# Kernel tuning notes

Hardware: AMD Instinct MI355X
Metric: run time of the kernel (lower is better)

The kernel has to match this reference:

```python
import jax, jax.numpy as jnp
import numpy as np

N_EMBED = 384
N_HEAD = 6
HEAD_SIZE = N_EMBED // N_HEAD  # 64
LN_EPS = 1e-5


def setup_inputs() -> dict:
    key = jax.random.key(0)
    ks = jax.random.split(key, 12)
    B, T = 128, 256
    s_in = 1.0 / np.sqrt(N_EMBED)
    s_ff = 1.0 / np.sqrt(4 * N_EMBED)
    return {
        "x": jax.random.normal(ks[0], (B, T, N_EMBED), jnp.float32),
        "Wq": jax.random.normal(ks[1], (N_HEAD, N_EMBED, HEAD_SIZE), jnp.float32) * s_in,
        "Wk": jax.random.normal(ks[2], (N_HEAD, N_EMBED, HEAD_SIZE), jnp.float32) * s_in,
        "Wv": jax.random.normal(ks[3], (N_HEAD, N_EMBED, HEAD_SIZE), jnp.float32) * s_in,
        "Wproj": jax.random.normal(ks[4], (N_EMBED, N_EMBED), jnp.float32) * s_in,
        "bproj": jnp.zeros((N_EMBED,), jnp.float32),
        "W1": jax.random.normal(ks[5], (N_EMBED, 4 * N_EMBED), jnp.float32) * s_in,
        "b1": jnp.zeros((4 * N_EMBED,), jnp.float32),
        "W2": jax.random.normal(ks[6], (4 * N_EMBED, N_EMBED), jnp.float32) * s_ff,
        "b2": jnp.zeros((N_EMBED,), jnp.float32),
        "ln1_g": jnp.ones((N_EMBED,), jnp.float32),
        "ln1_b": jnp.zeros((N_EMBED,), jnp.float32),
        "ln2_g": jnp.ones((N_EMBED,), jnp.float32),
        "ln2_b": jnp.zeros((N_EMBED,), jnp.float32),
    }


def _layernorm(x, g, b):
    mu = jnp.mean(x, axis=-1, keepdims=True)
    var = jnp.mean(jnp.square(x - mu), axis=-1, keepdims=True)
    return (x - mu) * jax.lax.rsqrt(var + LN_EPS) * g + b


def _attention(xn, Wq, Wk, Wv, Wproj, bproj):
    B, T, C = xn.shape
    q = jnp.einsum("btc,hcd->bhtd", xn, Wq)
    k = jnp.einsum("btc,hcd->bhtd", xn, Wk)
    v = jnp.einsum("btc,hcd->bhtd", xn, Wv)
    # NOTE: original scales by C**-0.5 with C = n_embed (384), not head_size
    scores = jnp.einsum("bhtd,bhsd->bhts", q, k) * (C ** -0.5)
    causal = jnp.tril(jnp.ones((T, T), bool))
    scores = jnp.where(causal, scores, -jnp.inf)
    wei = jax.nn.softmax(scores, axis=-1)
    out = jnp.einsum("bhts,bhsd->bhtd", wei, v)
    out = out.transpose(0, 2, 1, 3).reshape(B, T, N_EMBED)  # concat heads
    return out @ Wproj + bproj


def reference(x, Wq, Wk, Wv, Wproj, bproj, W1, b1, W2, b2, ln1_g, ln1_b, ln2_g, ln2_b):
    x = x + _attention(_layernorm(x, ln1_g, ln1_b), Wq, Wk, Wv, Wproj, bproj)
    h = _layernorm(x, ln2_g, ln2_b)
    ff = jax.nn.relu(h @ W1 + b1) @ W2 + b2
    return x + ff
```

## Files before the change

### kernel.cpp

```cpp
#include <hip/hip_runtime.h>
#include <hip/hip_bf16.h>

typedef __hip_bfloat16 bf16;
typedef __attribute__((ext_vector_type(8))) short bf16x8;
typedef __attribute__((ext_vector_type(4))) float f32x4;

#define CEMB 384
#define NHEAD 6
#define HSZ 64
#define TSEQ 256
#define BATCH 128
#define MROWS (BATCH*TSEQ)
#define FDIM 1536
#define QSCALE 0.05103103630798288f
#define SMAX 8.0f

#define AS1 __attribute__((address_space(1)))
#define AS3 __attribute__((address_space(3)))
__device__ __forceinline__ void gload16(const void* g, void* l){
  __builtin_amdgcn_global_load_lds((const AS1 unsigned*)(g), (AS3 unsigned*)(l), 16, 0, 0);
}
__device__ __forceinline__ float b2f(unsigned short u){
  unsigned int xi = ((unsigned int)u)<<16; float f; __builtin_memcpy(&f,&xi,4); return f;
}

__global__ __launch_bounds__(256) void ln_kernel(const float* __restrict__ x,
    const float* __restrict__ gam, const float* __restrict__ bet,
    bf16* __restrict__ y)
{
  const int row  = blockIdx.x*4 + (threadIdx.x>>6);
  const int lane = threadIdx.x & 63;
  const float* xr = x + (size_t)row*CEMB;
  float v[6]; float s = 0.f;
  #pragma unroll
  for (int i=0;i<6;i++){ v[i] = xr[lane + i*64]; s += v[i]; }
  #pragma unroll
  for (int m=1;m<64;m<<=1) s += __shfl_xor(s, m, 64);
  const float mu = s * (1.0f/CEMB);
  float qs = 0.f;
  #pragma unroll
  for (int i=0;i<6;i++){ v[i] -= mu; qs += v[i]*v[i]; }
  #pragma unroll
  for (int m=1;m<64;m<<=1) qs += __shfl_xor(qs, m, 64);
  const float rs = rsqrtf(qs*(1.0f/CEMB) + 1e-5f);
  bf16* yr = y + (size_t)row*CEMB;
  #pragma unroll
  for (int i=0;i<6;i++){
    int c = lane + i*64;
    yr[c] = __float2bfloat16(v[i]*rs*gam[c] + bet[c]);
  }
}

__global__ __launch_bounds__(256) void ln_kernel_b(const bf16* __restrict__ x,
    const float* __restrict__ gam, const float* __restrict__ bet,
    bf16* __restrict__ y)
{
  const int row  = blockIdx.x*4 + (threadIdx.x>>6);
  const int lane = threadIdx.x & 63;
  const ushort2* xr = (const ushort2*)(x + (size_t)row*CEMB);
  float v[6]; float s = 0.f;
  #pragma unroll
  for (int i=0;i<3;i++){
    ushort2 u = xr[lane + i*64];
    v[2*i]   = b2f(u.x); v[2*i+1] = b2f(u.y);
    s += v[2*i] + v[2*i+1];
  }
  #pragma unroll
  for (int m=1;m<64;m<<=1) s += __shfl_xor(s, m, 64);
  const float mu = s * (1.0f/CEMB);
  float qs = 0.f;
  #pragma unroll
  for (int i=0;i<6;i++){ v[i] -= mu; qs += v[i]*v[i]; }
  #pragma unroll
  for (int m=1;m<64;m<<=1) qs += __shfl_xor(qs, m, 64);
  const float rs = rsqrtf(qs*(1.0f/CEMB) + 1e-5f);
  bf16* yr = y + (size_t)row*CEMB;
  #pragma unroll
  for (int i=0;i<3;i++)
    #pragma unroll
    for (int j=0;j<2;j++){
      int c = (lane + i*64)*2 + j;
      yr[c] = __float2bfloat16(v[2*i+j]*rs*gam[c] + bet[c]);
    }
}

__global__ __launch_bounds__(256) void transpose_to_bf16(const float* __restrict__ src,
    bf16* __restrict__ dst, int K, int N)
{
  __shared__ float tile[32][33];
  const int n0 = blockIdx.x*32, k0 = blockIdx.y*32;
  src += (size_t)blockIdx.z*K*N;
  dst += (size_t)blockIdx.z*K*N;
  const int c = threadIdx.x & 31, r8 = threadIdx.x >> 5;
  #pragma unroll
  for (int i=0;i<4;i++)
    tile[r8 + i*8][c] = src[(size_t)(k0 + r8 + i*8)*N + n0 + c];
  __syncthreads();
  #pragma unroll
  for (int i=0;i<4;i++)
    dst[(size_t)(n0 + r8 + i*8)*K + k0 + c] = __float2bfloat16(tile[c][r8 + i*8]);
}

__global__ __launch_bounds__(256) void transpose_qkv(const float* __restrict__ Wq,
    const float* __restrict__ Wk, const float* __restrict__ Wv, bf16* __restrict__ dst)
{
  __shared__ float tile[32][33];
  const int z = blockIdx.z;
  const float* src = (z < 6) ? Wq : (z < 12 ? Wk : Wv);
  src += (size_t)(z % 6) * CEMB * HSZ;
  dst += (size_t)z * CEMB * HSZ;
  const int n0 = blockIdx.x*32, k0 = blockIdx.y*32;
  const int c = threadIdx.x & 31, r8 = threadIdx.x >> 5;
  #pragma unroll
  for (int i=0;i<4;i++)
    tile[r8 + i*8][c] = src[(size_t)(k0 + r8 + i*8)*HSZ + n0 + c];
  __syncthreads();
  #pragma unroll
  for (int i=0;i<4;i++)
    dst[(size_t)(n0 + r8 + i*8)*CEMB + k0 + c] = __float2bfloat16(tile[c][r8 + i*8]);
}

template<int EPI, int NN, int NK>
__global__ __launch_bounds__(512) void gemm2(
    const bf16* __restrict__ A, const bf16* __restrict__ BT,
    const float* __restrict__ bias, const float* __restrict__ resid,
    float* __restrict__ outf, bf16* __restrict__ outb0,
    bf16* __restrict__ outb1, bf16* __restrict__ outb2)
{
  constexpr int K = NK*32;
  constexpr int N = NN*128;
  __shared__ char lA[2][256*64];
  __shared__ char lB[2][128*64];
  const int cpx = gridDim.x >> 3;
  const int wg  = (blockIdx.x & 7)*cpx + (blockIdx.x >> 3);
  const int bm = (wg / NN)*256, bn = (wg % NN)*128;
  const int t = threadIdx.x, lane = t & 63, wid = t >> 6;
  const int wr = (wid>>1)*64, wc = (wid&1)*64;
  const int g = lane >> 4, fr = lane & 15;
  const size_t rowK2 = (size_t)K*2;
  f32x4 acc[4][4] = {};

  auto stage = [&](int buf, int kt){
    const size_t ko = (size_t)kt*64;
    #pragma unroll
    for (int i=0;i<2;i++){
      int slot = t + i*512;
      int row = slot>>2, blk = slot&3;
      gload16((const char*)A + (size_t)(bm+row)*rowK2 + ko + ((blk ^ ((row>>1)&3))<<4),
              lA[buf] + slot*16);
    }
    {
      int row = t>>2, blk = t&3;
      gload16((const char*)BT + (size_t)(bn+row)*rowK2 + ko + ((blk ^ ((row>>1)&3))<<4),
              lB[buf] + t*16);
    }
  };

  stage(0, 0);
  __syncthreads();
  int cur = 0;
  #pragma unroll 1
  for (int kt=0; kt<NK; ++kt){
    if (kt+1 < NK) stage(cur^1, kt+1);
    bf16x8 af[4], bq[4];
    #pragma unroll
    for (int mi=0;mi<4;mi++){
      int row = wr + mi*16 + fr;
      af[mi] = *(const bf16x8*)(lA[cur] + row*64 + ((g ^ ((row>>1)&3))<<4));
    }
    #pragma unroll
    for (int nj=0;nj<4;nj++){
      int row = wc + nj*16 + fr;
      bq[nj] = *(const bf16x8*)(lB[cur] + row*64 + ((g ^ ((row>>1)&3))<<4));
    }
    __builtin_amdgcn_s_setprio(1);
    #pragma unroll
    for (int mi=0;mi<4;mi++)
      #pragma unroll
      for (int nj=0;nj<4;nj++)
        acc[mi][nj] = __builtin_amdgcn_mfma_f32_16x16x32_bf16(af[mi], bq[nj], acc[mi][nj], 0, 0, 0);
    __builtin_amdgcn_s_setprio(0);
    __syncthreads();
    cur ^= 1;
  }

  if constexpr (EPI==0){
    const int sel = bn/CEMB;
    bf16* dst = sel==0 ? outb0 : (sel==1 ? outb1 : outb2);
    const float sc = sel==0 ? QSCALE : 1.0f;
    const int nb = bn - sel*CEMB;
    #pragma unroll
    for (int nj=0;nj<4;nj++){
      const int nn = nb + wc + nj*16 + fr;
      const int hh = nn>>6, dd = nn&63;
      #pragma unroll
      for (int mi=0;mi<4;mi++){
        const int m0 = bm + wr + mi*16 + 4*g;
        const int bb = m0>>8, tt0 = m0&255;
        bf16* p = dst + ((size_t)(bb*NHEAD + hh)*TSEQ + tt0)*HSZ + dd;
        #pragma unroll
        for (int e=0;e<4;e++)
          p[(size_t)e*HSZ] = __float2bfloat16(acc[mi][nj][e]*sc);
      }
    }
  } else {
    #pragma unroll
    for (int mi=0;mi<4;mi++)
      #pragma unroll
      for (int nj=0;nj<4;nj++)
        #pragma unroll
        for (int e=0;e<4;e++){
          const int m = bm + wr + mi*16 + 4*g + e;
          const int n = bn + wc + nj*16 + fr;
          const float vacc = acc[mi][nj][e];
          if constexpr (EPI==1){
            outb0[(size_t)m*N + n] = __float2bfloat16(vacc + bias[n] + resid[(size_t)m*N + n]);
          } else {
            float z = vacc + bias[n];
            outb0[(size_t)m*N + n] = __float2bfloat16(z > 0.f ? z : 0.f);
          }
        }
  }
}

template<int EPI, int NREAL, int NPAD, int NK>
__global__ __launch_bounds__(512, 2) void gemm8p(
    const bf16* __restrict__ A, const bf16* __restrict__ BT,
    const float* __restrict__ bias, const bf16* __restrict__ residb,
    float* __restrict__ outf)
{
  constexpr int K = NK*64;
  constexpr int NT = NPAD/256;
  __shared__ char lds[131072];
  const int cpx = gridDim.x >> 3;
  const int wg  = (blockIdx.x & 7)*cpx + (blockIdx.x >> 3);
  const int bm = (wg / NT)*256, bn = (wg % NT)*256;
  const int t = threadIdx.x, lane = t & 63, wid = t >> 6;
  const int wm = wid >> 2, wn = wid & 3;
  const int g = lane >> 4, fr = lane & 15;
  const size_t rowb = (size_t)K*2;
  const int sblk = ((t&3) ^ ((t>>3)&3)) << 4;
  const int swz  = (g ^ ((fr>>1)&3)) << 4;
  f32x4 acc[8][4] = {};

  const char* Ag = (const char*)A  + (size_t)(bm + (t>>2))*rowb + sblk;
  const char* Bg = (const char*)BT + (size_t)(bn + (t>>2))*rowb + sblk;
  const size_t rstep = rowb*128;

  auto stg = [&](int X, int KH, int sl, int kt2){
    const char* src = (X ? Bg : Ag) + (size_t)kt2*128 + KH*64;
    char* dst = lds + X*65536 + (KH*2+sl)*16384 + wid*1024;
    gload16(src,         dst);
    gload16(src + rstep, dst + 8192);
  };
  auto rdA = [&](bf16x8* af, int sl, int MH, int KS){
    const char* p = lds + (KS*2+sl)*16384 + (wm*128 + MH*64 + fr)*64 + swz;
    #pragma unroll
    for (int mi=0;mi<4;mi++) af[mi] = *(const bf16x8*)(p + mi*1024);
  };
  auto rdB = [&](bf16x8* bq, int sl, int KS){
    const char* p = lds + 65536 + (KS*2+sl)*16384 + (wn*64 + fr)*64 + swz;
    #pragma unroll
    for (int nj=0;nj<4;nj++) bq[nj] = *(const bf16x8*)(p + nj*1024);
  };

#define MFMA16(MH) \
  __builtin_amdgcn_s_setprio(1); \
  _Pragma("unroll") \
  for (int mi=0;mi<4;mi++){ \
    _Pragma("unroll") \
    for (int nj=0;nj<4;nj++) \
      acc[(MH)*4+mi][nj] = __builtin_amdgcn_mfma_f32_16x16x32_bf16(af[mi], bq[nj], acc[(MH)*4+mi][nj], 0, 0, 0); \
  } \
  __builtin_amdgcn_s_setprio(0);

  stg(0,0,0,0); stg(1,0,0,0); stg(0,1,0,0); stg(1,1,0,0);
  asm volatile("s_waitcnt vmcnt(4)" ::: "memory");
  __builtin_amdgcn_s_barrier();

  #pragma unroll 1
  for (int kt=0; kt<NK; ++kt){
    const int sl = kt&1, sn = sl^1;
    const bool pf = (kt+1 < NK);
    bf16x8 af[4], bq[4];
    rdA(af, sl, 0, 0); rdB(bq, sl, 0);
    if (pf) stg(0,0,sn,kt+1);
    __builtin_amdgcn_s_barrier();
    asm volatile("s_waitcnt lgkmcnt(0)" ::: "memory");
    __builtin_amdgcn_sched_barrier(0);
    MFMA16(0)
    __builtin_amdgcn_s_barrier();
    rdA(af, sl, 1, 0);
    if (pf){ stg(1,0,sn,kt+1);
             asm volatile("s_waitcnt vmcnt(4)" ::: "memory"); }
    else     asm volatile("s_waitcnt vmcnt(0)" ::: "memory");
    __builtin_amdgcn_s_barrier();
    asm volatile("s_waitcnt lgkmcnt(0)" ::: "memory");
    __builtin_amdgcn_sched_barrier(0);
    MFMA16(1)
    __builtin_amdgcn_s_barrier();
    rdA(af, sl, 0, 1); rdB(bq, sl, 1);
    if (pf) stg(0,1,sn,kt+1);
    __builtin_amdgcn_s_barrier();
    asm volatile("s_waitcnt lgkmcnt(0)" ::: "memory");
    __builtin_amdgcn_sched_barrier(0);
    MFMA16(0)
    __builtin_amdgcn_s_barrier();
    rdA(af, sl, 1, 1);
    if (pf){ stg(1,1,sn,kt+1);
             asm volatile("s_waitcnt vmcnt(4)" ::: "memory"); }
    __builtin_amdgcn_s_barrier();
    asm volatile("s_waitcnt lgkmcnt(0)" ::: "memory");
    __builtin_amdgcn_sched_barrier(0);
    MFMA16(1)
    __builtin_amdgcn_s_barrier();
  }
#undef MFMA16

  #pragma unroll
  for (int mi=0;mi<8;mi++)
    #pragma unroll
    for (int nj=0;nj<4;nj++)
      #pragma unroll
      for (int e=0;e<4;e++){
        const int m = bm + wm*128 + mi*16 + 4*g + e;
        const int n = bn + wn*64 + nj*16 + fr;
        if (NPAD == NREAL || n < NREAL){
          const float vacc = acc[mi][nj][e];
          outf[(size_t)m*NREAL + n] = vacc + bias[n] +
              b2f(*(const unsigned short*)&residb[(size_t)m*NREAL + n]);
        }
      }
}

__global__ __launch_bounds__(256) void attn_kernel(
    const bf16* __restrict__ q, const bf16* __restrict__ k,
    const bf16* __restrict__ v, bf16* __restrict__ out)
{
  __shared__ char kt_lds[64*128];
  __shared__ char vt_lds[80*128];
  __shared__ char p_lds[4][64*128];
  const int bh = blockIdx.x;
  const int bidx = bh / NHEAD, hidx = bh - bidx*NHEAD;
  const int t = threadIdx.x, lane = t & 63, w = t >> 6;
  const int g = lane >> 4, fr = lane & 15;
  const int lrow = lane >> 3;
  const int scol = ((lane & 7) ^ lrow) << 4;
  const size_t base = (size_t)bh * TSEQ * HSZ;

  if (t < 128){
    unsigned int ones2 = 0x3F803F80u;
    uint4 vv;
    if ((t>>3) == 0) vv = uint4{ones2, ones2, ones2, ones2};
    else             vv = uint4{0u, 0u, 0u, 0u};
    *(uint4*)(vt_lds + (64 + (t>>3))*128 + (t&7)*16) = vv;
  }

  bf16x8 qf[4][2];
  #pragma unroll
  for (int mi=0;mi<4;mi++)
    #pragma unroll
    for (int ks=0;ks<2;ks++)
      qf[mi][ks] = *(const bf16x8*)(q + base + (size_t)(w*64 + mi*16 + fr)*HSZ + ks*32 + g*8);

  f32x4 of[4][5] = {};

  for (int j=0;j<4;j++){
    __syncthreads();
    #pragma unroll
    for (int i=0;i<2;i++){
      int r0 = w*16 + i*8;
      gload16((const char*)(k + base + (size_t)(j*64 + r0 + lrow)*HSZ) + scol,
              kt_lds + r0*128);
    }
    #pragma unroll
    for (int i=0;i<2;i++){
      int chunk = t + i*256, r = chunk>>3, c = chunk&7;
      uint4 vv = *(const uint4*)(v + base + (size_t)(j*64 + r)*HSZ + c*8);
      const unsigned short* pv = (const unsigned short*)&vv;
      #pragma unroll
      for (int u=0;u<8;u++)
        *(unsigned short*)(vt_lds + (c*8+u)*128 + ((((r>>3) ^ u ^ c)&7)<<4) + (r&7)*2) = pv[u];
    }
    __syncthreads();
    if (j <= w){
      f32x4 sa[4][4] = {};
      #pragma unroll
      for (int ks=0;ks<2;ks++){
        bf16x8 kf[4];
        #pragma unroll
        for (int nj=0;nj<4;nj++)
          kf[nj] = *(const bf16x8*)(kt_lds + (nj*16+fr)*128 + (((ks*4+g)*16) ^ ((fr&7)<<4)));
        __builtin_amdgcn_s_setprio(1);
        #pragma unroll
        for (int mi=0;mi<4;mi++)
          #pragma unroll
          for (int nj=0;nj<4;nj++)
            sa[mi][nj] = __builtin_amdgcn_mfma_f32_16x16x32_bf16(qf[mi][ks], kf[nj], sa[mi][nj], 0, 0, 0);
        __builtin_amdgcn_s_setprio(0);
      }
      if (j == w){
        #pragma unroll
        for (int mi=0;mi<4;mi++)
          #pragma unroll
          for (int nj=0;nj<4;nj++)
            #pragma unroll
            for (int e=0;e<4;e++)
              if (nj*16 + fr > mi*16 + 4*g + e) sa[mi][nj][e] = -1e30f;
      }
      char* pl = p_lds[w];
      #pragma unroll
      for (int mi=0;mi<4;mi++)
        #pragma unroll
        for (int nj=0;nj<4;nj++)
          #pragma unroll
          for (int e=0;e<4;e++){
            int row = mi*16 + 4*g + e, col = nj*16 + fr;
            float p = __expf(sa[mi][nj][e] - SMAX);
            *(bf16*)(pl + row*128 + (((col>>3) ^ (row&7))<<4) + (col&7)*2) =
                __float2bfloat16(p);
          }
      #pragma unroll
      for (int ks=0;ks<2;ks++){
        bf16x8 pa[4], vf[5];
        #pragma unroll
        for (int mi=0;mi<4;mi++)
          pa[mi] = *(const bf16x8*)(pl + (mi*16+fr)*128 + (((ks*4+g)*16) ^ ((fr&7)<<4)));
        #pragma unroll
        for (int nd=0;nd<5;nd++){
          int d = nd*16 + fr;
          vf[nd] = *(const bf16x8*)(vt_lds + d*128 +
                   ((((ks*4+g) ^ (d&7) ^ ((d>>3)&7))&7)<<4));
        }
        __builtin_amdgcn_s_setprio(1);
        #pragma unroll
        for (int mi=0;mi<4;mi++)
          #pragma unroll
          for (int nd=0;nd<5;nd++)
            of[mi][nd] = __builtin_amdgcn_mfma_f32_16x16x32_bf16(pa[mi], vf[nd], of[mi][nd], 0, 0, 0);
        __builtin_amdgcn_s_setprio(0);
      }
    }
  }
  #pragma unroll
  for (int mi=0;mi<4;mi++){
    float rl[4];
    #pragma unroll
    for (int e=0;e<4;e++){
      float l = __shfl(of[mi][4][e], (int)(lane & 48), 64);
      rl[e] = 1.0f / l;
    }
    #pragma unroll
    for (int nd=0;nd<4;nd++)
      #pragma unroll
      for (int e=0;e<4;e++){
        int row = w*64 + mi*16 + 4*g + e;
        int d = nd*16 + fr;
        out[(size_t)(bidx*TSEQ + row)*CEMB + hidx*HSZ + d] =
            __float2bfloat16(of[mi][nd][e] * rl[e]);
      }
  }
}

extern "C" void kernel_launch(void* const* d_in, const int* in_sizes, int n_in,
                              void* d_out, int out_size, void* d_ws, size_t ws_size,
                              hipStream_t stream)
{
  const float* x     = (const float*)d_in[0];
  const float* Wq    = (const float*)d_in[1];
  const float* Wk    = (const float*)d_in[2];
  const float* Wv    = (const float*)d_in[3];
  const float* Wproj = (const float*)d_in[4];
  const float* bproj = (const float*)d_in[5];
  const float* W1    = (const float*)d_in[6];
  const float* b1    = (const float*)d_in[7];
  const float* W2    = (const float*)d_in[8];
  const float* b2    = (const float*)d_in[9];
  const float* ln1g  = (const float*)d_in[10];
  const float* ln1b  = (const float*)d_in[11];
  const float* ln2g  = (const float*)d_in[12];
  const float* ln2b  = (const float*)d_in[13];

  char* ws = (char*)d_ws;
  const size_t SA = (size_t)MROWS*CEMB*2;
  bf16* xn1    = (bf16*)(ws + 0*SA);
  bf16* qb     = (bf16*)(ws + 1*SA);
  bf16* kbuf   = (bf16*)(ws + 2*SA);
  bf16* vb     = (bf16*)(ws + 3*SA);
  bf16* attn_o = (bf16*)(ws + 0*SA);
  bf16* act    = (bf16*)(ws + 0*SA);
  bf16* hb     = (bf16*)(ws + 4*SA);
  bf16* x1b    = (bf16*)(ws + 5*SA);
  char* wb     = ws + 5*SA + (size_t)MROWS*CEMB*4;
  bf16* qkvT   = (bf16*)wb;
  bf16* projT  = (bf16*)(wb + (size_t)1152*384*2);
  bf16* w1T    = (bf16*)(wb + (size_t)(1152+384)*384*2);
  bf16* w2T    = (bf16*)(wb + (size_t)(1152+384+1536)*384*2);

  dim3 blk(256), blk5(512);
  transpose_qkv<<<dim3(2,12,18), blk, 0, stream>>>(Wq, Wk, Wv, qkvT);
  transpose_to_bf16<<<dim3(12,12,1), blk, 0, stream>>>(Wproj, projT, CEMB, CEMB);
  transpose_to_bf16<<<dim3(48,12,1), blk, 0, stream>>>(W1,    w1T,   CEMB, FDIM);
  transpose_to_bf16<<<dim3(12,48,1), blk, 0, stream>>>(W2,    w2T,   FDIM, CEMB);

  ln_kernel<<<dim3(MROWS/4), blk, 0, stream>>>(x, ln1g, ln1b, xn1);
  gemm2<0,9,12><<<dim3(1152), blk5, 0, stream>>>(xn1, qkvT, nullptr, nullptr,
                                                 nullptr, qb, kbuf, vb);
  attn_kernel<<<dim3(768), blk, 0, stream>>>(qb, kbuf, vb, attn_o);
  gemm2<1,3,12><<<dim3(384), blk5, 0, stream>>>(attn_o, projT, bproj, x,
                                                nullptr, x1b, nullptr, nullptr);
  ln_kernel_b<<<dim3(MROWS/4), blk, 0, stream>>>(x1b, ln2g, ln2b, hb);
  gemm2<2,12,12><<<dim3(1536), blk5, 0, stream>>>(hb, w1T, b1, nullptr,
                                                  nullptr, act, nullptr, nullptr);
  gemm8p<3,384,512,24><<<dim3(256), blk5, 0, stream>>>(act, w2T, b2, x1b, (float*)d_out);
}
```

Baseline: 261.5 us.

## Replace padded 256x256 W2 GEMM with 256x128 tiles and 3-stage pipeline

The final FFN down-projection GEMM used 256x256 tiles with N padded from 384 to 512, which wasted a quarter of its MFMA work. It now uses 256x128 tiles, so 384 divides exactly, with 384 workgroups and a triple-buffered LDS pipeline that prefetches two k-steps ahead. The LDS layout also changes to 128-byte rows with an XOR swizzle. The cost is 144KB of LDS per block, which allows only one block per CU, and each block reuses fewer loaded values per MFMA.

```diff
diff --git a/kernel.cpp b/kernel.cpp
--- a/kernel.cpp
+++ b/kernel.cpp
@@ -223,113 +223,106 @@
   }
 }
 
-template<int EPI, int NREAL, int NPAD, int NK>
-__global__ __launch_bounds__(512, 2) void gemm8p(
+template<int NK>
+__global__ __launch_bounds__(512) void gemm4p(
     const bf16* __restrict__ A, const bf16* __restrict__ BT,
     const float* __restrict__ bias, const bf16* __restrict__ residb,
     float* __restrict__ outf)
 {
   constexpr int K = NK*64;
-  constexpr int NT = NPAD/256;
-  __shared__ char lds[131072];
+  __shared__ char lds[147456];
   const int cpx = gridDim.x >> 3;
   const int wg  = (blockIdx.x & 7)*cpx + (blockIdx.x >> 3);
-  const int bm = (wg / NT)*256, bn = (wg % NT)*256;
+  const int bm = (wg/3)*256, bn = (wg%3)*128;
   const int t = threadIdx.x, lane = t & 63, wid = t >> 6;
-  const int wm = wid >> 2, wn = wid & 3;
+  const int wm = wid >> 1, wn = wid & 1;
   const int g = lane >> 4, fr = lane & 15;
   const size_t rowb = (size_t)K*2;
-  const int sblk = ((t&3) ^ ((t>>3)&3)) << 4;
-  const int swz  = (g ^ ((fr>>1)&3)) << 4;
-  f32x4 acc[8][4] = {};
-
-  const char* Ag = (const char*)A  + (size_t)(bm + (t>>2))*rowb + sblk;
-  const char* Bg = (const char*)BT + (size_t)(bn + (t>>2))*rowb + sblk;
-  const size_t rstep = rowb*128;
-
-  auto stg = [&](int X, int KH, int sl, int kt2){
-    const char* src = (X ? Bg : Ag) + (size_t)kt2*128 + KH*64;
-    char* dst = lds + X*65536 + (KH*2+sl)*16384 + wid*1024;
-    gload16(src,         dst);
-    gload16(src + rstep, dst + 8192);
+  f32x4 acc[4][4] = {};
+
+  auto stgA = [&](int c, int sl, int kt2){
+    #pragma unroll
+    for (int j=0;j<2;j++){
+      int slot = t + j*512;
+      int row = slot>>3, blk = slot&7;
+      gload16((const char*)A + (size_t)(bm + c*128 + row)*rowb + (size_t)kt2*128 + ((blk ^ (row&7))<<4),
+              lds + sl*32768 + c*16384 + j*8192 + wid*1024);
+    }
   };
-  auto rdA = [&](bf16x8* af, int sl, int MH, int KS){
-    const char* p = lds + (KS*2+sl)*16384 + (wm*128 + MH*64 + fr)*64 + swz;
-    #pragma unroll
-    for (int mi=0;mi<4;mi++) af[mi] = *(const bf16x8*)(p + mi*1024);
+  auto stgB = [&](int sl, int kt2){
+    #pragma unroll
+    for (int j=0;j<2;j++){
+      int slot = t + j*512;
+      int row = slot>>3, blk = slot&7;
+      gload16((const char*)BT + (size_t)(bn + row)*rowb + (size_t)kt2*128 + ((blk ^ (row&7))<<4),
+              lds + 98304 + sl*16384 + j*8192 + wid*1024);
+    }
   };
-  auto rdB = [&](bf16x8* bq, int sl, int KS){
-    const char* p = lds + 65536 + (KS*2+sl)*16384 + (wn*64 + fr)*64 + swz;
-    #pragma unroll
-    for (int nj=0;nj<4;nj++) bq[nj] = *(const bf16x8*)(p + nj*1024);
+  auto rdA = [&](bf16x8* af, int sl, int ks){
+    #pragma unroll
+    for (int mi=0;mi<4;mi++){
+      int row = wm*64 + mi*16 + fr;
+      af[mi] = *(const bf16x8*)(lds + sl*32768 + row*128 + (((ks*4+g) ^ (row&7))<<4));
+    }
   };
-
-#define MFMA16(MH) \
+  auto rdB = [&](bf16x8* bq, int sl, int ks){
+    #pragma unroll
+    for (int nj=0;nj<4;nj++){
+      int row = wn*64 + nj*16 + fr;
+      bq[nj] = *(const bf16x8*)(lds + 98304 + sl*16384 + row*128 + (((ks*4+g) ^ (row&7))<<4));
+    }
+  };
+
+#define MFMA16_4P \
   __builtin_amdgcn_s_setprio(1); \
   _Pragma("unroll") \
   for (int mi=0;mi<4;mi++){ \
     _Pragma("unroll") \
     for (int nj=0;nj<4;nj++) \
-      acc[(MH)*4+mi][nj] = __builtin_amdgcn_mfma_f32_16x16x32_bf16(af[mi], bq[nj], acc[(MH)*4+mi][nj], 0, 0, 0); \
+      acc[mi][nj] = __builtin_amdgcn_mfma_f32_16x16x32_bf16(af[mi], bq[nj], acc[mi][nj], 0, 0, 0); \
   } \
   __builtin_amdgcn_s_setprio(0);
 
-  stg(0,0,0,0); stg(1,0,0,0); stg(0,1,0,0); stg(1,1,0,0);
-  asm volatile("s_waitcnt vmcnt(4)" ::: "memory");
+  stgA(0,0,0); stgA(1,0,0); stgB(0,0);
+  stgA(0,1,1); stgA(1,1,1); stgB(1,1);
+  asm volatile("s_waitcnt vmcnt(6)" ::: "memory");
   __builtin_amdgcn_s_barrier();
 
   #pragma unroll 1
   for (int kt=0; kt<NK; ++kt){
-    const int sl = kt&1, sn = sl^1;
-    const bool pf = (kt+1 < NK);
+    const int sl = kt%3, s2 = (kt+2)%3;
+    const bool pf = (kt+2 < NK);
     bf16x8 af[4], bq[4];
-    rdA(af, sl, 0, 0); rdB(bq, sl, 0);
-    if (pf) stg(0,0,sn,kt+1);
+    rdA(af, sl, 0); rdB(bq, sl, 0);
+    if (pf){ stgA(0,s2,kt+2); stgA(1,s2,kt+2); }
     __builtin_amdgcn_s_barrier();
     asm volatile("s_waitcnt lgkmcnt(0)" ::: "memory");
     __builtin_amdgcn_sched_barrier(0);
-    MFMA16(0)
+    MFMA16_4P
     __builtin_amdgcn_s_barrier();
-    rdA(af, sl, 1, 0);
-    if (pf){ stg(1,0,sn,kt+1);
-             asm volatile("s_waitcnt vmcnt(4)" ::: "memory"); }
-    else     asm volatile("s_waitcnt vmcnt(0)" ::: "memory");
+    rdA(af, sl, 1); rdB(bq, sl, 1);
+    if (pf){ stgB(s2, kt+2);
+             asm volatile("s_waitcnt vmcnt(6)" ::: "memory"); }
+    else if (kt+1 < NK)
+             asm volatile("s_waitcnt vmcnt(0)" ::: "memory");
     __builtin_amdgcn_s_barrier();
     asm volatile("s_waitcnt lgkmcnt(0)" ::: "memory");
     __builtin_amdgcn_sched_barrier(0);
-    MFMA16(1)
+    MFMA16_4P
     __builtin_amdgcn_s_barrier();
-    rdA(af, sl, 0, 1); rdB(bq, sl, 1);
-    if (pf) stg(0,1,sn,kt+1);
-    __builtin_amdgcn_s_barrier();
-    asm volatile("s_waitcnt lgkmcnt(0)" ::: "memory");
-    __builtin_amdgcn_sched_barrier(0);
-    MFMA16(0)
-    __builtin_amdgcn_s_barrier();
-    rdA(af, sl, 1, 1);
-    if (pf){ stg(1,1,sn,kt+1);
-             asm volatile("s_waitcnt vmcnt(4)" ::: "memory"); }
-    __builtin_amdgcn_s_barrier();
-    asm volatile("s_waitcnt lgkmcnt(0)" ::: "memory");
-    __builtin_amdgcn_sched_barrier(0);
-    MFMA16(1)
-    __builtin_amdgcn_s_barrier();
-  }
-#undef MFMA16
-
-  #pragma unroll
-  for (int mi=0;mi<8;mi++)
+  }
+#undef MFMA16_4P
+
+  #pragma unroll
+  for (int mi=0;mi<4;mi++)
     #pragma unroll
     for (int nj=0;nj<4;nj++)
       #pragma unroll
       for (int e=0;e<4;e++){
-        const int m = bm + wm*128 + mi*16 + 4*g + e;
+        const int m = bm + wm*64 + mi*16 + 4*g + e;
         const int n = bn + wn*64 + nj*16 + fr;
-        if (NPAD == NREAL || n < NREAL){
-          const float vacc = acc[mi][nj][e];
-          outf[(size_t)m*NREAL + n] = vacc + bias[n] +
-              b2f(*(const unsigned short*)&residb[(size_t)m*NREAL + n]);
-        }
+        outf[(size_t)m*CEMB + n] = acc[mi][nj][e] + bias[n] +
+            b2f(*(const unsigned short*)&residb[(size_t)m*CEMB + n]);
       }
 }
 
@@ -512,5 +505,5 @@
   ln_kernel_b<<<dim3(MROWS/4), blk, 0, stream>>>(x1b, ln2g, ln2b, hb);
   gemm2<2,12,12><<<dim3(1536), blk5, 0, stream>>>(hb, w1T, b1, nullptr,
                                                   nullptr, act, nullptr, nullptr);
-  gemm8p<3,384,512,24><<<dim3(256), blk5, 0, stream>>>(act, w2T, b2, x1b, (float*)d_out);
-}
+  gemm4p<24><<<dim3(384), blk5, 0, stream>>>(act, w2T, b2, x1b, (float*)d_out);
+}
```

Result: no change. 264.8 us (+1.3%).

## Use 256x192 tiles in FFN down-projection GEMM to eliminate N padding

Applied to the files above, without the earlier changes.

Replaces the padded 256x256 tile GEMM (N padded from 384 to 512) with a 256x192 tile variant that covers N=384 exactly with two column tiles. B staging is restructured with a new swizzled LDS layout and three loads per thread, and wait counts are re-tuned. This removes the MFMA work and B traffic spent on padding columns, at the cost of a less square tile with lower per-tile reuse.

```diff
diff --git a/kernel.cpp b/kernel.cpp
--- a/kernel.cpp
+++ b/kernel.cpp
@@ -223,113 +223,118 @@
   }
 }
 
-template<int EPI, int NREAL, int NPAD, int NK>
-__global__ __launch_bounds__(512, 2) void gemm8p(
+template<int NK>
+__global__ __launch_bounds__(512, 2) void gemm8n(
     const bf16* __restrict__ A, const bf16* __restrict__ BT,
     const float* __restrict__ bias, const bf16* __restrict__ residb,
     float* __restrict__ outf)
 {
   constexpr int K = NK*64;
-  constexpr int NT = NPAD/256;
-  __shared__ char lds[131072];
+  __shared__ char lds[114688];
   const int cpx = gridDim.x >> 3;
   const int wg  = (blockIdx.x & 7)*cpx + (blockIdx.x >> 3);
-  const int bm = (wg / NT)*256, bn = (wg % NT)*256;
+  const int bm = (wg >> 1)*256, bn = (wg & 1)*192;
   const int t = threadIdx.x, lane = t & 63, wid = t >> 6;
   const int wm = wid >> 2, wn = wid & 3;
   const int g = lane >> 4, fr = lane & 15;
   const size_t rowb = (size_t)K*2;
-  const int sblk = ((t&3) ^ ((t>>3)&3)) << 4;
-  const int swz  = (g ^ ((fr>>1)&3)) << 4;
-  f32x4 acc[8][4] = {};
-
-  const char* Ag = (const char*)A  + (size_t)(bm + (t>>2))*rowb + sblk;
-  const char* Bg = (const char*)BT + (size_t)(bn + (t>>2))*rowb + sblk;
+  const int sblkA = ((t&3) ^ ((t>>3)&3)) << 4;
+  const int swzA  = (g ^ ((fr>>1)&3)) << 4;
+  f32x4 acc[8][3] = {};
+
+  const char* Ag = (const char*)A + (size_t)(bm + (t>>2))*rowb + sblkA;
   const size_t rstep = rowb*128;
 
-  auto stg = [&](int X, int KH, int sl, int kt2){
-    const char* src = (X ? Bg : Ag) + (size_t)kt2*128 + KH*64;
-    char* dst = lds + X*65536 + (KH*2+sl)*16384 + wid*1024;
+  auto stgA = [&](int KH, int sl, int kt2){
+    const char* src = Ag + (size_t)kt2*128 + KH*64;
+    char* dst = lds + sl*32768 + KH*16384 + wid*1024;
     gload16(src,         dst);
     gload16(src + rstep, dst + 8192);
   };
+  auto stgB = [&](int sl, int kt2){
+    #pragma unroll
+    for (int j=0;j<3;j++){
+      int slot = t + j*512;
+      int row = slot>>3, blk = slot&7;
+      gload16((const char*)BT + (size_t)(bn + row)*rowb + (size_t)kt2*128 + ((blk ^ (row&7))<<4),
+              lds + 65536 + sl*24576 + j*8192 + wid*1024);
+    }
+  };
   auto rdA = [&](bf16x8* af, int sl, int MH, int KS){
-    const char* p = lds + (KS*2+sl)*16384 + (wm*128 + MH*64 + fr)*64 + swz;
+    const char* p = lds + sl*32768 + KS*16384 + (wm*128 + MH*64 + fr)*64 + swzA;
     #pragma unroll
     for (int mi=0;mi<4;mi++) af[mi] = *(const bf16x8*)(p + mi*1024);
   };
-  auto rdB = [&](bf16x8* bq, int sl, int KS){
-    const char* p = lds + 65536 + (KS*2+sl)*16384 + (wn*64 + fr)*64 + swz;
-    #pragma unroll
-    for (int nj=0;nj<4;nj++) bq[nj] = *(const bf16x8*)(p + nj*1024);
+  auto rdB = [&](bf16x8* bq, int sl, int ks){
+    #pragma unroll
+    for (int nj=0;nj<3;nj++){
+      int row = wn*48 + nj*16 + fr;
+      bq[nj] = *(const bf16x8*)(lds + 65536 + sl*24576 + row*128 + (((ks*4+g) ^ (row&7))<<4));
+    }
   };
 
-#define MFMA16(MH) \
+#define MFMA12(MH) \
   __builtin_amdgcn_s_setprio(1); \
   _Pragma("unroll") \
   for (int mi=0;mi<4;mi++){ \
     _Pragma("unroll") \
-    for (int nj=0;nj<4;nj++) \
+    for (int nj=0;nj<3;nj++) \
       acc[(MH)*4+mi][nj] = __builtin_amdgcn_mfma_f32_16x16x32_bf16(af[mi], bq[nj], acc[(MH)*4+mi][nj], 0, 0, 0); \
   } \
   __builtin_amdgcn_s_setprio(0);
 
-  stg(0,0,0,0); stg(1,0,0,0); stg(0,1,0,0); stg(1,1,0,0);
-  asm volatile("s_waitcnt vmcnt(4)" ::: "memory");
+  stgA(0,0,0); stgB(0,0); stgA(1,0,0);
+  asm volatile("s_waitcnt vmcnt(2)" ::: "memory");
   __builtin_amdgcn_s_barrier();
 
   #pragma unroll 1
   for (int kt=0; kt<NK; ++kt){
     const int sl = kt&1, sn = sl^1;
     const bool pf = (kt+1 < NK);
-    bf16x8 af[4], bq[4];
+    bf16x8 af[4], bq[3];
     rdA(af, sl, 0, 0); rdB(bq, sl, 0);
-    if (pf) stg(0,0,sn,kt+1);
+    if (pf) stgA(0,sn,kt+1);
     __builtin_amdgcn_s_barrier();
     asm volatile("s_waitcnt lgkmcnt(0)" ::: "memory");
     __builtin_amdgcn_sched_barrier(0);
-    MFMA16(0)
+    MFMA12(0)
     __builtin_amdgcn_s_barrier();
     rdA(af, sl, 1, 0);
-    if (pf){ stg(1,0,sn,kt+1);
-             asm volatile("s_waitcnt vmcnt(4)" ::: "memory"); }
+    if (pf){ stgB(sn,kt+1);
+             asm volatile("s_waitcnt vmcnt(5)" ::: "memory"); }
     else     asm volatile("s_waitcnt vmcnt(0)" ::: "memory");
     __builtin_amdgcn_s_barrier();
     asm volatile("s_waitcnt lgkmcnt(0)" ::: "memory");
     __builtin_amdgcn_sched_barrier(0);
-    MFMA16(1)
+    MFMA12(1)
     __builtin_amdgcn_s_barrier();
     rdA(af, sl, 0, 1); rdB(bq, sl, 1);
-    if (pf) stg(0,1,sn,kt+1);
+    if (pf) stgA(1,sn,kt+1);
     __builtin_amdgcn_s_barrier();
     asm volatile("s_waitcnt lgkmcnt(0)" ::: "memory");
     __builtin_amdgcn_sched_barrier(0);
-    MFMA16(0)
+    MFMA12(0)
     __builtin_amdgcn_s_barrier();
     rdA(af, sl, 1, 1);
-    if (pf){ stg(1,1,sn,kt+1);
-             asm volatile("s_waitcnt vmcnt(4)" ::: "memory"); }
+    if (pf) asm volatile("s_waitcnt vmcnt(2)" ::: "memory");
     __builtin_amdgcn_s_barrier();
     asm volatile("s_waitcnt lgkmcnt(0)" ::: "memory");
     __builtin_amdgcn_sched_barrier(0);
-    MFMA16(1)
-    __builtin_amdgcn_s_barrier();
-  }
-#undef MFMA16
+    MFMA12(1)
+    __builtin_amdgcn_s_barrier();
+  }
+#undef MFMA12
 
   #pragma unroll
   for (int mi=0;mi<8;mi++)
     #pragma unroll
-    for (int nj=0;nj<4;nj++)
+    for (int nj=0;nj<3;nj++)
       #pragma unroll
       for (int e=0;e<4;e++){
         const int m = bm + wm*128 + mi*16 + 4*g + e;
-        const int n = bn + wn*64 + nj*16 + fr;
-        if (NPAD == NREAL || n < NREAL){
-          const float vacc = acc[mi][nj][e];
-          outf[(size_t)m*NREAL + n] = vacc + bias[n] +
-              b2f(*(const unsigned short*)&residb[(size_t)m*NREAL + n]);
-        }
+        const int n = bn + wn*48 + nj*16 + fr;
+        outf[(size_t)m*CEMB + n] = acc[mi][nj][e] + bias[n] +
+            b2f(*(const unsigned short*)&residb[(size_t)m*CEMB + n]);
       }
 }
 
@@ -512,5 +517,5 @@
   ln_kernel_b<<<dim3(MROWS/4), blk, 0, stream>>>(x1b, ln2g, ln2b, hb);
   gemm2<2,12,12><<<dim3(1536), blk5, 0, stream>>>(hb, w1T, b1, nullptr,
                                                   nullptr, act, nullptr, nullptr);
-  gemm8p<3,384,512,24><<<dim3(256), blk5, 0, stream>>>(act, w2T, b2, x1b, (float*)d_out);
-}
+  gemm8n<24><<<dim3(256), blk5, 0, stream>>>(act, w2T, b2, x1b, (float*)d_out);
+}
```

After: 250.9 us. 1.04x faster.
